# Performance work log

Measured on AMD Instinct MI355X. Metric: run time of the kernel, lower is better.

Reference implementation:

```python
import jax, jax.numpy as jnp
import numpy as np

BATCH, IN_DIM, OUT_DIM = 512, 1024, 1024

def setup_inputs() -> dict:
    key = jax.random.key(0)
    kx, kw = jax.random.split(key)
    x = jax.random.normal(kx, (BATCH, IN_DIM), dtype=jnp.float32)
    W = jax.random.normal(kw, (OUT_DIM, IN_DIM), dtype=jnp.float32)
    return {"x": x, "W": W}

def reference(x, W):
    # Tropical (max-plus) matmul: y[b,o] = max_i (x[b,i] + W[o,i])
    # x: [B, I], W: [O, I] -> y: [B, O]
    return jnp.max(x[:, None, :] + W[None, :, :], axis=-1)
```

## Files before the change

kernel.cpp:

```cpp
#include <hip/hip_runtime.h>
#include <math.h>


#define MDIM 512
#define NDIM 1024
#define KDIM 1024

#define BM 64
#define BN 64
#define BK 32
#define PAD 4
#define TM 4
#define TN 4
#define NTHREADS 256

__global__ __launch_bounds__(NTHREADS)
void tropical_partial(const float* __restrict__ x, const float* __restrict__ W,
                      float* __restrict__ ws, int KC) {
    __shared__ float As[BK][BM + PAD];
    __shared__ float Bs[BK][BN + PAD];

    const int tiles_n = NDIM / BN;
    const int tile    = blockIdx.x;
    const int tm0     = (tile / tiles_n) * BM;
    const int tn0     = (tile % tiles_n) * BN;
    const int k0      = blockIdx.y * KC;

    const int tid = threadIdx.x;
    const int sm = tid >> 2;
    const int sk = (tid & 3) * 8;
    const int tx = tid & 15;
    const int ty = tid >> 4;

    float acc[TM][TN];
#pragma unroll
    for (int i = 0; i < TM; ++i)
#pragma unroll
        for (int j = 0; j < TN; ++j) acc[i][j] = -INFINITY;

    for (int kt = 0; kt < KC; kt += BK) {
        const int kb = k0 + kt;
        const float4 a0 = *(const float4*)&x[(size_t)(tm0 + sm) * KDIM + kb + sk];
        const float4 a1 = *(const float4*)&x[(size_t)(tm0 + sm) * KDIM + kb + sk + 4];
        const float4 b0 = *(const float4*)&W[(size_t)(tn0 + sm) * KDIM + kb + sk];
        const float4 b1 = *(const float4*)&W[(size_t)(tn0 + sm) * KDIM + kb + sk + 4];

        __syncthreads();
        As[sk + 0][sm] = a0.x; As[sk + 1][sm] = a0.y;
        As[sk + 2][sm] = a0.z; As[sk + 3][sm] = a0.w;
        As[sk + 4][sm] = a1.x; As[sk + 5][sm] = a1.y;
        As[sk + 6][sm] = a1.z; As[sk + 7][sm] = a1.w;
        Bs[sk + 0][sm] = b0.x; Bs[sk + 1][sm] = b0.y;
        Bs[sk + 2][sm] = b0.z; Bs[sk + 3][sm] = b0.w;
        Bs[sk + 4][sm] = b1.x; Bs[sk + 5][sm] = b1.y;
        Bs[sk + 6][sm] = b1.z; Bs[sk + 7][sm] = b1.w;
        __syncthreads();

#pragma unroll 8
        for (int kk = 0; kk < BK; ++kk) {
            const float4 av = *(const float4*)&As[kk][ty * TM];
            const float4 bv = *(const float4*)&Bs[kk][tx * TN];
            const float a[4] = {av.x, av.y, av.z, av.w};
            const float b[4] = {bv.x, bv.y, bv.z, bv.w};
#pragma unroll
            for (int i = 0; i < TM; ++i)
#pragma unroll
                for (int j = 0; j < TN; ++j)
                    acc[i][j] = fmaxf(acc[i][j], a[i] + b[j]);
        }
    }

    float* wsl = ws + (size_t)blockIdx.y * MDIM * NDIM;
#pragma unroll
    for (int i = 0; i < TM; ++i) {
        const float4 v = make_float4(acc[i][0], acc[i][1], acc[i][2], acc[i][3]);
        *(float4*)&wsl[(size_t)(tm0 + ty * TM + i) * NDIM + tn0 + tx * TN] = v;
    }
}

__global__ __launch_bounds__(NTHREADS)
void tropical_reduce(const float* __restrict__ ws, float* __restrict__ out, int KS) {
    const int i = blockIdx.x * NTHREADS + threadIdx.x;
    const int stride = MDIM * NDIM / 4;
    if (i >= stride) return;
    const float4* w4 = (const float4*)ws;
    float4 m = w4[i];
    for (int s = 1; s < KS; ++s) {
        const float4 v = w4[(size_t)s * stride + i];
        m.x = fmaxf(m.x, v.x); m.y = fmaxf(m.y, v.y);
        m.z = fmaxf(m.z, v.z); m.w = fmaxf(m.w, v.w);
    }
    ((float4*)out)[i] = m;
}

extern "C" void kernel_launch(void* const* d_in, const int* in_sizes, int n_in,
                              void* d_out, int out_size, void* d_ws, size_t ws_size,
                              hipStream_t stream) {
    const float* x = (const float*)d_in[0];
    const float* W = (const float*)d_in[1];
    float* out = (float*)d_out;
    float* ws  = (float*)d_ws;

    const size_t slice = (size_t)MDIM * NDIM * sizeof(float);
    int KS = 8;
    while (KS > 1 && (size_t)KS * slice > ws_size) KS >>= 1;

    const int ntiles = (MDIM / BM) * (NDIM / BN);

    if ((size_t)KS * slice > ws_size) {
        tropical_partial<<<dim3(ntiles, 1), NTHREADS, 0, stream>>>(x, W, out, KDIM);
        return;
    }

    const int KC = KDIM / KS;
    tropical_partial<<<dim3(ntiles, KS), NTHREADS, 0, stream>>>(x, W, ws, KC);

    const int nvec4 = MDIM * NDIM / 4;
    tropical_reduce<<<(nvec4 + NTHREADS - 1) / NTHREADS, NTHREADS, 0, stream>>>(ws, out, KS);
}
```

Measured before the change: 86.61 us.

## Enlarge tropical matmul tiles to 128x128 with double-buffered LDS and packed adds

Each block now covers a 128x128 output tile with an 8x8 per-thread register tile instead of 64x64 with 4x4. Shared memory is double-buffered: the next K-slice is loaded from global memory while the current one is being computed. The LDS layout interleaves k-pairs so the inner loop can issue two-wide packed float adds and then two max ops per accumulator. The aim is more reuse per LDS load and less exposed global latency. In exchange the launch has a quarter as many tiles, lower occupancy from launch_bounds(256,1), and much higher register pressure.

Result: slower. 127.3 us (+47.0%).

```diff
diff --git a/kernel.cpp b/kernel.cpp
--- a/kernel.cpp
+++ b/kernel.cpp
@@ -6,29 +6,32 @@
 #define NDIM 1024
 #define KDIM 1024
 
-#define BM 64
-#define BN 64
+#define BM 128
+#define BN 128
 #define BK 32
-#define PAD 4
-#define TM 4
-#define TN 4
+#define KPR 16
+#define STR 256
+#define TM 8
+#define TN 8
 #define NTHREADS 256
 
-__global__ __launch_bounds__(NTHREADS)
+typedef float v2f __attribute__((ext_vector_type(2)));
+
+__global__ __launch_bounds__(NTHREADS, 1)
 void tropical_partial(const float* __restrict__ x, const float* __restrict__ W,
                       float* __restrict__ ws, int KC) {
-    __shared__ float As[BK][BM + PAD];
-    __shared__ float Bs[BK][BN + PAD];
+    __shared__ float As[2][KPR][STR];
+    __shared__ float Bs[2][KPR][STR];
 
     const int tiles_n = NDIM / BN;
-    const int tile    = blockIdx.x;
-    const int tm0     = (tile / tiles_n) * BM;
-    const int tn0     = (tile % tiles_n) * BN;
-    const int k0      = blockIdx.y * KC;
+    const int tm0 = (blockIdx.x / tiles_n) * BM;
+    const int tn0 = (blockIdx.x % tiles_n) * BM;
+    const int k0  = blockIdx.y * KC;
 
     const int tid = threadIdx.x;
-    const int sm = tid >> 2;
-    const int sk = (tid & 3) * 8;
+    const int sm = tid >> 1;
+    const int sk = (tid & 1) * 16;
+    const int sp = sk >> 1;
     const int tx = tid & 15;
     const int ty = tid >> 4;
 
@@ -38,44 +41,93 @@
 #pragma unroll
         for (int j = 0; j < TN; ++j) acc[i][j] = -INFINITY;
 
-    for (int kt = 0; kt < KC; kt += BK) {
-        const int kb = k0 + kt;
-        const float4 a0 = *(const float4*)&x[(size_t)(tm0 + sm) * KDIM + kb + sk];
-        const float4 a1 = *(const float4*)&x[(size_t)(tm0 + sm) * KDIM + kb + sk + 4];
-        const float4 b0 = *(const float4*)&W[(size_t)(tn0 + sm) * KDIM + kb + sk];
-        const float4 b1 = *(const float4*)&W[(size_t)(tn0 + sm) * KDIM + kb + sk + 4];
+    const float* xrow = x + (size_t)(tm0 + sm) * KDIM + sk;
+    const float* wrow = W + (size_t)(tn0 + sm) * KDIM + sk;
 
-        __syncthreads();
-        As[sk + 0][sm] = a0.x; As[sk + 1][sm] = a0.y;
-        As[sk + 2][sm] = a0.z; As[sk + 3][sm] = a0.w;
-        As[sk + 4][sm] = a1.x; As[sk + 5][sm] = a1.y;
-        As[sk + 6][sm] = a1.z; As[sk + 7][sm] = a1.w;
-        Bs[sk + 0][sm] = b0.x; Bs[sk + 1][sm] = b0.y;
-        Bs[sk + 2][sm] = b0.z; Bs[sk + 3][sm] = b0.w;
-        Bs[sk + 4][sm] = b1.x; Bs[sk + 5][sm] = b1.y;
-        Bs[sk + 6][sm] = b1.z; Bs[sk + 7][sm] = b1.w;
+    float4 a[4], b[4];
+    {
+        const float4* xp = (const float4*)(xrow + k0);
+        const float4* wp = (const float4*)(wrow + k0);
+        a[0] = xp[0]; a[1] = xp[1]; a[2] = xp[2]; a[3] = xp[3];
+        b[0] = wp[0]; b[1] = wp[1]; b[2] = wp[2]; b[3] = wp[3];
+    }
+#define WRITE_TILE(bf)                                              \
+    {                                                               \
+        _Pragma("unroll")                                           \
+        for (int q = 0; q < 4; ++q) {                               \
+            v2f lo, hi;                                             \
+            lo.x = a[q].x; lo.y = a[q].y;                           \
+            hi.x = a[q].z; hi.y = a[q].w;                           \
+            *(v2f*)&As[bf][sp + 2 * q + 0][2 * sm] = lo;            \
+            *(v2f*)&As[bf][sp + 2 * q + 1][2 * sm] = hi;            \
+            lo.x = b[q].x; lo.y = b[q].y;                           \
+            hi.x = b[q].z; hi.y = b[q].w;                           \
+            *(v2f*)&Bs[bf][sp + 2 * q + 0][2 * sm] = lo;            \
+            *(v2f*)&Bs[bf][sp + 2 * q + 1][2 * sm] = hi;            \
+        }                                                           \
+    }
+    WRITE_TILE(0)
+
+    const int nt = KC / BK;
+    for (int t = 0; t < nt; ++t) {
+        const int cur = t & 1;
+        if (t + 1 < nt) {
+            const float4* xp = (const float4*)(xrow + k0 + (t + 1) * BK);
+            const float4* wp = (const float4*)(wrow + k0 + (t + 1) * BK);
+            a[0] = xp[0]; a[1] = xp[1]; a[2] = xp[2]; a[3] = xp[3];
+            b[0] = wp[0]; b[1] = wp[1]; b[2] = wp[2]; b[3] = wp[3];
+        }
         __syncthreads();
 
-#pragma unroll 8
-        for (int kk = 0; kk < BK; ++kk) {
-            const float4 av = *(const float4*)&As[kk][ty * TM];
-            const float4 bv = *(const float4*)&Bs[kk][tx * TN];
-            const float a[4] = {av.x, av.y, av.z, av.w};
-            const float b[4] = {bv.x, bv.y, bv.z, bv.w};
+        const float4* Ap = ((const float4*)As[cur]) + ty * 4;
+        const float4* Bp = ((const float4*)Bs[cur]) + tx;
+#pragma unroll
+        for (int kp = 0; kp < KPR; ++kp) {
+            const float4 af0 = Ap[kp * 64 + 0];
+            const float4 af1 = Ap[kp * 64 + 1];
+            const float4 af2 = Ap[kp * 64 + 2];
+            const float4 af3 = Ap[kp * 64 + 3];
+            const float4 bf0 = Bp[kp * 64 + 0];
+            const float4 bf1 = Bp[kp * 64 + 16];
+            const float4 bf2 = Bp[kp * 64 + 32];
+            const float4 bf3 = Bp[kp * 64 + 48];
+            v2f am[TM], bn[TN];
+            am[0].x = af0.x; am[0].y = af0.y;  am[1].x = af0.z; am[1].y = af0.w;
+            am[2].x = af1.x; am[2].y = af1.y;  am[3].x = af1.z; am[3].y = af1.w;
+            am[4].x = af2.x; am[4].y = af2.y;  am[5].x = af2.z; am[5].y = af2.w;
+            am[6].x = af3.x; am[6].y = af3.y;  am[7].x = af3.z; am[7].y = af3.w;
+            bn[0].x = bf0.x; bn[0].y = bf0.y;  bn[1].x = bf0.z; bn[1].y = bf0.w;
+            bn[2].x = bf1.x; bn[2].y = bf1.y;  bn[3].x = bf1.z; bn[3].y = bf1.w;
+            bn[4].x = bf2.x; bn[4].y = bf2.y;  bn[5].x = bf2.z; bn[5].y = bf2.w;
+            bn[6].x = bf3.x; bn[6].y = bf3.y;  bn[7].x = bf3.z; bn[7].y = bf3.w;
 #pragma unroll
             for (int i = 0; i < TM; ++i)
 #pragma unroll
-                for (int j = 0; j < TN; ++j)
-                    acc[i][j] = fmaxf(acc[i][j], a[i] + b[j]);
+                for (int j = 0; j < TN; ++j) {
+                    const v2f s = am[i] + bn[j];
+                    acc[i][j] = fmaxf(fmaxf(acc[i][j], s.x), s.y);
+                }
+        }
+
+        if (t + 1 < nt) {
+            const int nxt = cur ^ 1;
+            WRITE_TILE(nxt)
         }
     }
 
-    float* wsl = ws + (size_t)blockIdx.y * MDIM * NDIM;
+    float* wsl = ws + (size_t)blockIdx.y * (MDIM * NDIM);
 #pragma unroll
     for (int i = 0; i < TM; ++i) {
-        const float4 v = make_float4(acc[i][0], acc[i][1], acc[i][2], acc[i][3]);
-        *(float4*)&wsl[(size_t)(tm0 + ty * TM + i) * NDIM + tn0 + tx * TN] = v;
+        float* r = &wsl[(size_t)(tm0 + ty * TM + i) * NDIM + tn0 + 2 * tx];
+#pragma unroll
+        for (int jj = 0; jj < 4; ++jj) {
+            v2f v;
+            v.x = acc[i][2 * jj];
+            v.y = acc[i][2 * jj + 1];
+            *(v2f*)(r + 32 * jj) = v;
+        }
     }
+#undef WRITE_TILE
 }
 
 __global__ __launch_bounds__(NTHREADS)
```

## Use 64-thread blocks with 8x8 register tiles, packed v2f adds and register prefetch

Applied to the files above, without the earlier changes.

Rewrites the partial kernel so each 64-thread block computes a 64x64 tile with 8x8 outputs per thread, which raises register reuse. LDS gets a swizzled k-pair layout so packed two-wide float adds (v2f) can be used. The next K tile is prefetched into registers while the current one is computed, and the split-K factor goes from 8 to 16. The gains are fewer LDS reads per max-plus op and wider packed arithmetic, paid for with heavier register pressure, a larger workspace to reduce, and only one wave per block.

New measurement: 91.31 us. 5.4% more time.

```diff
diff --git a/kernel.cpp b/kernel.cpp
--- a/kernel.cpp
+++ b/kernel.cpp
@@ -6,85 +6,119 @@
 #define NDIM 1024
 #define KDIM 1024
 
-#define BM 64
-#define BN 64
+#define TILE 64
 #define BK 32
-#define PAD 4
-#define TM 4
-#define TN 4
-#define NTHREADS 256
+#define KPR (BK / 2)
+#define CH 33
+#define ROWF (CH * 4)
+#define NTHREADS 64
 
-__global__ __launch_bounds__(NTHREADS)
+typedef float v2f __attribute__((ext_vector_type(2)));
+
+__device__ __forceinline__ int swz(int c) { return c ^ (c >> 2); }
+
+__global__ __launch_bounds__(NTHREADS, 2)
 void tropical_partial(const float* __restrict__ x, const float* __restrict__ W,
                       float* __restrict__ ws, int KC) {
-    __shared__ float As[BK][BM + PAD];
-    __shared__ float Bs[BK][BN + PAD];
+    __shared__ float As[KPR * ROWF];
+    __shared__ float Bs[KPR * ROWF];
 
-    const int tiles_n = NDIM / BN;
-    const int tile    = blockIdx.x;
-    const int tm0     = (tile / tiles_n) * BM;
-    const int tn0     = (tile % tiles_n) * BN;
-    const int k0      = blockIdx.y * KC;
+    const int tiles_n = NDIM / TILE;
+    const int tm0 = (blockIdx.x / tiles_n) * TILE;
+    const int tn0 = (blockIdx.x % tiles_n) * TILE;
+    const int k0  = blockIdx.y * KC;
 
-    const int tid = threadIdx.x;
-    const int sm = tid >> 2;
-    const int sk = (tid & 3) * 8;
-    const int tx = tid & 15;
-    const int ty = tid >> 4;
+    const int l  = threadIdx.x;
+    const int q  = l & 7;
+    const int r0 = l >> 3;
+    const int tx = q, ty = r0;
 
-    float acc[TM][TN];
+    float acc[8][8];
 #pragma unroll
-    for (int i = 0; i < TM; ++i)
+    for (int i = 0; i < 8; ++i)
 #pragma unroll
-        for (int j = 0; j < TN; ++j) acc[i][j] = -INFINITY;
+        for (int j = 0; j < 8; ++j) acc[i][j] = -INFINITY;
 
-    for (int kt = 0; kt < KC; kt += BK) {
-        const int kb = k0 + kt;
-        const float4 a0 = *(const float4*)&x[(size_t)(tm0 + sm) * KDIM + kb + sk];
-        const float4 a1 = *(const float4*)&x[(size_t)(tm0 + sm) * KDIM + kb + sk + 4];
-        const float4 b0 = *(const float4*)&W[(size_t)(tn0 + sm) * KDIM + kb + sk];
-        const float4 b1 = *(const float4*)&W[(size_t)(tn0 + sm) * KDIM + kb + sk + 4];
+    const float* xb = x + (size_t)tm0 * KDIM + k0 + 4 * q;
+    const float* wb = W + (size_t)tn0 * KDIM + k0 + 4 * q;
 
-        __syncthreads();
-        As[sk + 0][sm] = a0.x; As[sk + 1][sm] = a0.y;
-        As[sk + 2][sm] = a0.z; As[sk + 3][sm] = a0.w;
-        As[sk + 4][sm] = a1.x; As[sk + 5][sm] = a1.y;
-        As[sk + 6][sm] = a1.z; As[sk + 7][sm] = a1.w;
-        Bs[sk + 0][sm] = b0.x; Bs[sk + 1][sm] = b0.y;
-        Bs[sk + 2][sm] = b0.z; Bs[sk + 3][sm] = b0.w;
-        Bs[sk + 4][sm] = b1.x; Bs[sk + 5][sm] = b1.y;
-        Bs[sk + 6][sm] = b1.z; Bs[sk + 7][sm] = b1.w;
-        __syncthreads();
+    float4 xg[8], wg[8];
+    const int nt = KC / BK;
 
-#pragma unroll 8
-        for (int kk = 0; kk < BK; ++kk) {
-            const float4 av = *(const float4*)&As[kk][ty * TM];
-            const float4 bv = *(const float4*)&Bs[kk][tx * TN];
-            const float a[4] = {av.x, av.y, av.z, av.w};
-            const float b[4] = {bv.x, bv.y, bv.z, bv.w};
 #pragma unroll
-            for (int i = 0; i < TM; ++i)
+    for (int j = 0; j < 8; ++j) {
+        xg[j] = *(const float4*)(xb + (size_t)(r0 + 8 * j) * KDIM);
+        wg[j] = *(const float4*)(wb + (size_t)(r0 + 8 * j) * KDIM);
+    }
+
+    for (int t = 0; t < nt; ++t) {
 #pragma unroll
-                for (int j = 0; j < TN; ++j)
-                    acc[i][j] = fmaxf(acc[i][j], a[i] + b[j]);
+        for (int j = 0; j < 8; ++j) {
+            const int ms  = r0 + 8 * j;
+            const int col = swz(ms >> 1) * 4 + (ms & 1) * 2;
+            v2f lo, hi;
+            lo.x = xg[j].x; lo.y = xg[j].y;
+            hi.x = xg[j].z; hi.y = xg[j].w;
+            *(v2f*)&As[(2 * q) * ROWF + col]     = lo;
+            *(v2f*)&As[(2 * q + 1) * ROWF + col] = hi;
+            lo.x = wg[j].x; lo.y = wg[j].y;
+            hi.x = wg[j].z; hi.y = wg[j].w;
+            *(v2f*)&Bs[(2 * q) * ROWF + col]     = lo;
+            *(v2f*)&Bs[(2 * q + 1) * ROWF + col] = hi;
+        }
+        if (t + 1 < nt) {
+            const float* xn = xb + (size_t)(t + 1) * BK;
+            const float* wn = wb + (size_t)(t + 1) * BK;
+#pragma unroll
+            for (int j = 0; j < 8; ++j) {
+                xg[j] = *(const float4*)(xn + (size_t)(r0 + 8 * j) * KDIM);
+                wg[j] = *(const float4*)(wn + (size_t)(r0 + 8 * j) * KDIM);
+            }
+        }
+#pragma unroll
+        for (int kp = 0; kp < KPR; ++kp) {
+            const float* ra = As + kp * ROWF;
+            const float* rb = Bs + kp * ROWF;
+            float4 af[4], bf[4];
+#pragma unroll
+            for (int qq = 0; qq < 4; ++qq) {
+                af[qq] = *(const float4*)(ra + ((4 * ty + qq) ^ ty) * 4);
+                bf[qq] = *(const float4*)(rb + ((4 * tx + qq) ^ tx) * 4);
+            }
+            v2f am[8], bn[8];
+#pragma unroll
+            for (int qq = 0; qq < 4; ++qq) {
+                am[2 * qq].x     = af[qq].x; am[2 * qq].y     = af[qq].y;
+                am[2 * qq + 1].x = af[qq].z; am[2 * qq + 1].y = af[qq].w;
+                bn[2 * qq].x     = bf[qq].x; bn[2 * qq].y     = bf[qq].y;
+                bn[2 * qq + 1].x = bf[qq].z; bn[2 * qq + 1].y = bf[qq].w;
+            }
+#pragma unroll
+            for (int i = 0; i < 8; ++i)
+#pragma unroll
+                for (int j = 0; j < 8; ++j) {
+                    const v2f s = am[i] + bn[j];
+                    acc[i][j] = fmaxf(fmaxf(acc[i][j], s.x), s.y);
+                }
         }
     }
 
-    float* wsl = ws + (size_t)blockIdx.y * MDIM * NDIM;
+    float* wsl = ws + (size_t)blockIdx.y * (MDIM * NDIM);
 #pragma unroll
-    for (int i = 0; i < TM; ++i) {
-        const float4 v = make_float4(acc[i][0], acc[i][1], acc[i][2], acc[i][3]);
-        *(float4*)&wsl[(size_t)(tm0 + ty * TM + i) * NDIM + tn0 + tx * TN] = v;
+    for (int i = 0; i < 8; ++i) {
+        float* r = &wsl[(size_t)(tm0 + 8 * ty + i) * NDIM + tn0 + 8 * tx];
+        *(float4*)(r)     = make_float4(acc[i][0], acc[i][1], acc[i][2], acc[i][3]);
+        *(float4*)(r + 4) = make_float4(acc[i][4], acc[i][5], acc[i][6], acc[i][7]);
     }
 }
 
-__global__ __launch_bounds__(NTHREADS)
+__global__ __launch_bounds__(256)
 void tropical_reduce(const float* __restrict__ ws, float* __restrict__ out, int KS) {
-    const int i = blockIdx.x * NTHREADS + threadIdx.x;
+    const int i = blockIdx.x * 256 + threadIdx.x;
     const int stride = MDIM * NDIM / 4;
-    if (i >= stride) return;
     const float4* w4 = (const float4*)ws;
     float4 m = w4[i];
+#pragma unroll 4
     for (int s = 1; s < KS; ++s) {
         const float4 v = w4[(size_t)s * stride + i];
         m.x = fmaxf(m.x, v.x); m.y = fmaxf(m.y, v.y);
@@ -102,12 +136,12 @@
     float* ws  = (float*)d_ws;
 
     const size_t slice = (size_t)MDIM * NDIM * sizeof(float);
-    int KS = 8;
+    int KS = 16;
     while (KS > 1 && (size_t)KS * slice > ws_size) KS >>= 1;
 
-    const int ntiles = (MDIM / BM) * (NDIM / BN);
+    const int ntiles = (MDIM / TILE) * (NDIM / TILE);
 
-    if ((size_t)KS * slice > ws_size) {
+    if (slice > ws_size) {
         tropical_partial<<<dim3(ntiles, 1), NTHREADS, 0, stream>>>(x, W, out, KDIM);
         return;
     }
@@ -116,5 +150,5 @@
     tropical_partial<<<dim3(ntiles, KS), NTHREADS, 0, stream>>>(x, W, ws, KC);
 
     const int nvec4 = MDIM * NDIM / 4;
-    tropical_reduce<<<(nvec4 + NTHREADS - 1) / NTHREADS, NTHREADS, 0, stream>>>(ws, out, KS);
+    tropical_reduce<<<nvec4 / 256, 256, 0, stream>>>(ws, out, KS);
 }
```

## Transpose inputs into k-pair-major layout and compute max-plus with packed float2 adds

Applied to the files above, without the earlier changes.

Adds pre-pass kernels that transpose x and W into a k-pair-major layout of float2 pairs. The main kernel then drops shared memory and has each wavefront cover 16 rows by 64 columns. Each lane keeps its W column in registers with a prefetch buffer, while the x values are wave-uniform loads. Packed two-wide adds are meant to halve the add instruction count, and the split-K factor rises to 16. The cost is two extra transpose launches, more workspace, more partial-result traffic in the reduce, and a naive fallback kernel.

New measurement: 141.6 us. 63.5% more time.

```diff
diff --git a/kernel.cpp b/kernel.cpp
--- a/kernel.cpp
+++ b/kernel.cpp
@@ -5,86 +5,75 @@
 #define MDIM 512
 #define NDIM 1024
 #define KDIM 1024
+#define KP2  (KDIM / 2)
+#define TMR  16
+#define DPF  4
 
-#define BM 64
-#define BN 64
-#define BK 32
-#define PAD 4
-#define TM 4
-#define TN 4
-#define NTHREADS 256
+typedef float v2f __attribute__((ext_vector_type(2)));
 
-__global__ __launch_bounds__(NTHREADS)
-void tropical_partial(const float* __restrict__ x, const float* __restrict__ W,
-                      float* __restrict__ ws, int KC) {
-    __shared__ float As[BK][BM + PAD];
-    __shared__ float Bs[BK][BN + PAD];
+__global__ __launch_bounds__(256)
+void pair_transpose(const v2f* __restrict__ in, v2f* __restrict__ out,
+                    int R, int C) {
+    __shared__ v2f t[32][33];
+    const int tx = threadIdx.x & 31, ty = threadIdx.x >> 5;
+    const int c0 = blockIdx.x * 32, r0 = blockIdx.y * 32;
+#pragma unroll
+    for (int j = 0; j < 4; ++j)
+        t[ty + 8 * j][tx] = in[(size_t)(r0 + ty + 8 * j) * C + c0 + tx];
+    __syncthreads();
+#pragma unroll
+    for (int j = 0; j < 4; ++j)
+        out[(size_t)(c0 + ty + 8 * j) * R + r0 + tx] = t[tx][ty + 8 * j];
+}
 
-    const int tiles_n = NDIM / BN;
-    const int tile    = blockIdx.x;
-    const int tm0     = (tile / tiles_n) * BM;
-    const int tn0     = (tile % tiles_n) * BN;
-    const int k0      = blockIdx.y * KC;
+__global__ __launch_bounds__(256, 4)
+void tropical_partial(const v2f* __restrict__ xP,
+                      const v2f* __restrict__ wP,
+                      float* __restrict__ part, int KCP) {
+    const int wid  = threadIdx.x >> 6;
+    const int lane = threadIdx.x & 63;
+    const int task = blockIdx.x * 4 + wid;
+    const int mb = task >> 4, nb = task & 15;
+    const int m0 = mb * TMR, n0 = nb * 64;
+    const int kp0 = blockIdx.y * KCP;
 
-    const int tid = threadIdx.x;
-    const int sm = tid >> 2;
-    const int sk = (tid & 3) * 8;
-    const int tx = tid & 15;
-    const int ty = tid >> 4;
+    float acc[TMR];
+#pragma unroll
+    for (int i = 0; i < TMR; ++i) acc[i] = -INFINITY;
 
-    float acc[TM][TN];
+    const v2f* wcol = wP + (size_t)kp0 * NDIM + n0 + lane;
+    const v2f* xrow = xP + (size_t)kp0 * MDIM + m0;
+
+    v2f wbuf[DPF];
 #pragma unroll
-    for (int i = 0; i < TM; ++i)
+    for (int d = 0; d < DPF; ++d) wbuf[d] = wcol[(size_t)d * NDIM];
+
+#pragma unroll 4
+    for (int kp = 0; kp < KCP; ++kp) {
+        const v2f w2 = wbuf[kp & (DPF - 1)];
+        if (kp + DPF < KCP)
+            wbuf[kp & (DPF - 1)] = wcol[(size_t)(kp + DPF) * NDIM];
+        const v2f* xr = xrow + (size_t)kp * MDIM;
 #pragma unroll
-        for (int j = 0; j < TN; ++j) acc[i][j] = -INFINITY;
-
-    for (int kt = 0; kt < KC; kt += BK) {
-        const int kb = k0 + kt;
-        const float4 a0 = *(const float4*)&x[(size_t)(tm0 + sm) * KDIM + kb + sk];
-        const float4 a1 = *(const float4*)&x[(size_t)(tm0 + sm) * KDIM + kb + sk + 4];
-        const float4 b0 = *(const float4*)&W[(size_t)(tn0 + sm) * KDIM + kb + sk];
-        const float4 b1 = *(const float4*)&W[(size_t)(tn0 + sm) * KDIM + kb + sk + 4];
-
-        __syncthreads();
-        As[sk + 0][sm] = a0.x; As[sk + 1][sm] = a0.y;
-        As[sk + 2][sm] = a0.z; As[sk + 3][sm] = a0.w;
-        As[sk + 4][sm] = a1.x; As[sk + 5][sm] = a1.y;
-        As[sk + 6][sm] = a1.z; As[sk + 7][sm] = a1.w;
-        Bs[sk + 0][sm] = b0.x; Bs[sk + 1][sm] = b0.y;
-        Bs[sk + 2][sm] = b0.z; Bs[sk + 3][sm] = b0.w;
-        Bs[sk + 4][sm] = b1.x; Bs[sk + 5][sm] = b1.y;
-        Bs[sk + 6][sm] = b1.z; Bs[sk + 7][sm] = b1.w;
-        __syncthreads();
-
-#pragma unroll 8
-        for (int kk = 0; kk < BK; ++kk) {
-            const float4 av = *(const float4*)&As[kk][ty * TM];
-            const float4 bv = *(const float4*)&Bs[kk][tx * TN];
-            const float a[4] = {av.x, av.y, av.z, av.w};
-            const float b[4] = {bv.x, bv.y, bv.z, bv.w};
-#pragma unroll
-            for (int i = 0; i < TM; ++i)
-#pragma unroll
-                for (int j = 0; j < TN; ++j)
-                    acc[i][j] = fmaxf(acc[i][j], a[i] + b[j]);
+        for (int i = 0; i < TMR; ++i) {
+            const v2f s = w2 + xr[i];
+            acc[i] = fmaxf(fmaxf(acc[i], s.x), s.y);
         }
     }
 
-    float* wsl = ws + (size_t)blockIdx.y * MDIM * NDIM;
+    float* dst = part + (size_t)blockIdx.y * (MDIM * NDIM);
 #pragma unroll
-    for (int i = 0; i < TM; ++i) {
-        const float4 v = make_float4(acc[i][0], acc[i][1], acc[i][2], acc[i][3]);
-        *(float4*)&wsl[(size_t)(tm0 + ty * TM + i) * NDIM + tn0 + tx * TN] = v;
-    }
+    for (int i = 0; i < TMR; ++i)
+        dst[(size_t)(m0 + i) * NDIM + n0 + lane] = acc[i];
 }
 
-__global__ __launch_bounds__(NTHREADS)
+__global__ __launch_bounds__(256)
 void tropical_reduce(const float* __restrict__ ws, float* __restrict__ out, int KS) {
-    const int i = blockIdx.x * NTHREADS + threadIdx.x;
+    const int i = blockIdx.x * 256 + threadIdx.x;
     const int stride = MDIM * NDIM / 4;
-    if (i >= stride) return;
     const float4* w4 = (const float4*)ws;
     float4 m = w4[i];
+#pragma unroll 4
     for (int s = 1; s < KS; ++s) {
         const float4 v = w4[(size_t)s * stride + i];
         m.x = fmaxf(m.x, v.x); m.y = fmaxf(m.y, v.y);
@@ -93,28 +82,52 @@
     ((float4*)out)[i] = m;
 }
 
+__global__ __launch_bounds__(256)
+void tropical_naive(const float* __restrict__ x, const float* __restrict__ W,
+                    float* __restrict__ out) {
+    const int idx = blockIdx.x * 256 + threadIdx.x;
+    const int b = idx >> 10, n = idx & 1023;
+    const float4* xr = (const float4*)(x + (size_t)b * KDIM);
+    const float4* wr = (const float4*)(W + (size_t)n * KDIM);
+    float m = -INFINITY;
+    for (int k = 0; k < KDIM / 4; ++k) {
+        const float4 a = xr[k], w = wr[k];
+        m = fmaxf(m, fmaxf(fmaxf(a.x + w.x, a.y + w.y),
+                           fmaxf(a.z + w.z, a.w + w.w)));
+    }
+    out[idx] = m;
+}
+
 extern "C" void kernel_launch(void* const* d_in, const int* in_sizes, int n_in,
                               void* d_out, int out_size, void* d_ws, size_t ws_size,
                               hipStream_t stream) {
     const float* x = (const float*)d_in[0];
     const float* W = (const float*)d_in[1];
     float* out = (float*)d_out;
-    float* ws  = (float*)d_ws;
 
+    const size_t xPsz  = (size_t)KP2 * MDIM * sizeof(v2f);
+    const size_t wPsz  = (size_t)KP2 * NDIM * sizeof(v2f);
     const size_t slice = (size_t)MDIM * NDIM * sizeof(float);
-    int KS = 8;
-    while (KS > 1 && (size_t)KS * slice > ws_size) KS >>= 1;
 
-    const int ntiles = (MDIM / BM) * (NDIM / BN);
+    int KS = 16;
+    while (KS > 1 && xPsz + wPsz + (size_t)KS * slice > ws_size) KS >>= 1;
 
-    if ((size_t)KS * slice > ws_size) {
-        tropical_partial<<<dim3(ntiles, 1), NTHREADS, 0, stream>>>(x, W, out, KDIM);
+    if (xPsz + wPsz + slice > ws_size) {
+        tropical_naive<<<MDIM * NDIM / 256, 256, 0, stream>>>(x, W, out);
         return;
     }
 
-    const int KC = KDIM / KS;
-    tropical_partial<<<dim3(ntiles, KS), NTHREADS, 0, stream>>>(x, W, ws, KC);
+    v2f*   xP   = (v2f*)d_ws;
+    v2f*   wP   = (v2f*)((char*)d_ws + xPsz);
+    float* part = (float*)((char*)d_ws + xPsz + wPsz);
 
-    const int nvec4 = MDIM * NDIM / 4;
-    tropical_reduce<<<(nvec4 + NTHREADS - 1) / NTHREADS, NTHREADS, 0, stream>>>(ws, out, KS);
+    pair_transpose<<<dim3(KP2 / 32, MDIM / 32), 256, 0, stream>>>(
+        (const v2f*)x, xP, MDIM, KP2);
+    pair_transpose<<<dim3(KP2 / 32, NDIM / 32), 256, 0, stream>>>(
+        (const v2f*)W, wP, NDIM, KP2);
+
+    const int KCP = KP2 / KS;
+    tropical_partial<<<dim3(128, KS), 256, 0, stream>>>(xP, wP, part, KCP);
+
+    tropical_reduce<<<MDIM * NDIM / 4 / 256, 256, 0, stream>>>(part, out, KS);
 }
```
